# Kernel tuning notes

Measured on AMD Instinct MI355X. Metric: run time of the kernel, lower is better.

Reference implementation:

```python
import jax, jax.numpy as jnp
import numpy as np

VOCAB = 100000
EMB = 300
B, L = 2048, 256

def setup_inputs() -> dict:
    key = jax.random.key(0)
    k1, k2, k3, k4 = jax.random.split(key, 4)
    tokens = jax.random.randint(k1, (B, L), 0, VOCAB)
    # lengths in [1, L] (original items always have at least one token)
    lengths = jax.random.randint(k2, (B,), 1, L + 1)
    W_emb = jax.random.normal(k3, (VOCAB, EMB), dtype=jnp.float32)
    fc_w = jax.random.normal(k4, (1, EMB), dtype=jnp.float32) / np.sqrt(EMB)
    fc_b = jnp.zeros((1,), dtype=jnp.float32)
    return {"tokens": tokens, "lengths": lengths, "W_emb": W_emb, "fc_w": fc_w, "fc_b": fc_b}

def reference(tokens, lengths, W_emb, fc_w, fc_b):
    # ragged gather + per-item mean pool, fused via padding mask
    emb = W_emb[tokens]                                   # [B, L, D]
    mask = (jnp.arange(L)[None, :] < lengths[:, None])    # [B, L]
    summed = jnp.einsum('bld,bl->bd', emb, mask.astype(emb.dtype))
    avg = summed / lengths[:, None].astype(emb.dtype)     # [B, D]
    z = avg @ fc_w.T + fc_b                               # [B, 1]
    return jax.nn.sigmoid(z)
```

## Files before the change

### kernel.cpp

```cpp
#include <hip/hip_runtime.h>
#include <hip/hip_bf16.h>

#define VOCAB 100000
#define EMB 300
#define BATCH 2048
#define SEQ 256

__global__ void __launch_bounds__(256) vocab_dot_kernel(
    const float* __restrict__ W, const float* __restrict__ fcw,
    float* __restrict__ p, int nrows) {
  const int lane = threadIdx.x & 63;
  const int wave = (blockIdx.x * blockDim.x + threadIdx.x) >> 6;
  const int nwaves = (gridDim.x * blockDim.x) >> 6;

  const float4* fcw4 = (const float4*)fcw;
  float4 wa = fcw4[lane];
  float4 wb = make_float4(0.f, 0.f, 0.f, 0.f);
  if (lane < 11) wb = fcw4[64 + lane];

  for (int v = wave * 2; v < nrows; v += nwaves * 2) {
    const float4* r0 = (const float4*)(W + (size_t)v * EMB);
    float4 a0 = r0[lane];
    float4 t0 = (lane < 11) ? r0[64 + lane] : make_float4(0.f, 0.f, 0.f, 0.f);
    float4 a1 = make_float4(0.f, 0.f, 0.f, 0.f);
    float4 t1 = make_float4(0.f, 0.f, 0.f, 0.f);
    const bool has1 = (v + 1) < nrows;
    if (has1) {
      const float4* r1 = (const float4*)(W + (size_t)(v + 1) * EMB);
      a1 = r1[lane];
      if (lane < 11) t1 = r1[64 + lane];
    }

    float acc0 = a0.x * wa.x + a0.y * wa.y + a0.z * wa.z + a0.w * wa.w
               + t0.x * wb.x + t0.y * wb.y + t0.z * wb.z + t0.w * wb.w;
    float acc1 = a1.x * wa.x + a1.y * wa.y + a1.z * wa.z + a1.w * wa.w
               + t1.x * wb.x + t1.y * wb.y + t1.z * wb.z + t1.w * wb.w;

    #pragma unroll
    for (int off = 32; off > 0; off >>= 1) {
      acc0 += __shfl_down(acc0, off, 64);
      acc1 += __shfl_down(acc1, off, 64);
    }
    if (lane == 0) {
      p[v] = acc0;
      if (has1) p[v + 1] = acc1;
    }
  }
}

__global__ void __launch_bounds__(256) pool_sigmoid_kernel(
    const int* __restrict__ tokens, const int* __restrict__ lengths,
    const float* __restrict__ p, const float* __restrict__ fcb,
    float* __restrict__ out, int L) {
  __shared__ float part[4];
  const int b = blockIdx.x;
  const int t = threadIdx.x;
  const int len = lengths[b];

  float acc = 0.f;
  if (t < len) acc = p[tokens[(size_t)b * L + t]];

  #pragma unroll
  for (int off = 32; off > 0; off >>= 1)
    acc += __shfl_down(acc, off, 64);

  const int lane = t & 63, w = t >> 6;
  if (lane == 0) part[w] = acc;
  __syncthreads();
  if (t == 0) {
    float s = part[0] + part[1] + part[2] + part[3];
    float z = s / (float)len + fcb[0];
    out[b] = 1.0f / (1.0f + expf(-z));
  }
}

extern "C" void kernel_launch(void* const* d_in, const int* in_sizes, int n_in,
                              void* d_out, int out_size, void* d_ws, size_t ws_size,
                              hipStream_t stream) {
  const int*   tokens  = (const int*)d_in[0];
  const int*   lengths = (const int*)d_in[1];
  const float* W_emb   = (const float*)d_in[2];
  const float* fc_w    = (const float*)d_in[3];
  const float* fc_b    = (const float*)d_in[4];
  float* out = (float*)d_out;
  float* p   = (float*)d_ws;

  vocab_dot_kernel<<<2048, 256, 0, stream>>>(W_emb, fc_w, p, VOCAB);

  pool_sigmoid_kernel<<<BATCH, 256, 0, stream>>>(
      tokens, lengths, p, fc_b, out, SEQ);
}
```

Measured before the change: 27.57 us.

## Process four vocab rows per wave with 16-lane groups and nontemporal loads

Each wave now splits into four 16-lane groups, and each group computes the dot product of one embedding row with fc_w. That replaces the old two-rows-per-wave mapping and its 6-step full-wave shuffle reductions with a 4-step 16-lane xor reduction. Each lane issues five 16-byte loads per row instead of one or two, and the loads are marked nontemporal so the streaming read of W does not pollute the cache. This raises memory-level parallelism per wave and cuts shuffle overhead. It adds more registers for the five weight vectors.

Result: faster. 26.92 us (-2.3%).

```diff
diff --git a/kernel.cpp b/kernel.cpp
--- a/kernel.cpp
+++ b/kernel.cpp
@@ -6,45 +6,43 @@
 #define BATCH 2048
 #define SEQ 256
 
+typedef float f4 __attribute__((ext_vector_type(4)));
+
 __global__ void __launch_bounds__(256) vocab_dot_kernel(
     const float* __restrict__ W, const float* __restrict__ fcw,
     float* __restrict__ p, int nrows) {
   const int lane = threadIdx.x & 63;
+  const int g    = lane >> 4;
+  const int i    = lane & 15;
   const int wave = (blockIdx.x * blockDim.x + threadIdx.x) >> 6;
   const int nwaves = (gridDim.x * blockDim.x) >> 6;
 
-  const float4* fcw4 = (const float4*)fcw;
-  float4 wa = fcw4[lane];
-  float4 wb = make_float4(0.f, 0.f, 0.f, 0.f);
-  if (lane < 11) wb = fcw4[64 + lane];
+  const f4* fcw4 = (const f4*)fcw;
+  const f4 zero = (f4){0.f, 0.f, 0.f, 0.f};
+  f4 w0 = fcw4[i];
+  f4 w1 = fcw4[i + 16];
+  f4 w2 = fcw4[i + 32];
+  f4 w3 = fcw4[i + 48];
+  f4 w4 = (i < 11) ? fcw4[i + 64] : zero;
 
-  for (int v = wave * 2; v < nrows; v += nwaves * 2) {
-    const float4* r0 = (const float4*)(W + (size_t)v * EMB);
-    float4 a0 = r0[lane];
-    float4 t0 = (lane < 11) ? r0[64 + lane] : make_float4(0.f, 0.f, 0.f, 0.f);
-    float4 a1 = make_float4(0.f, 0.f, 0.f, 0.f);
-    float4 t1 = make_float4(0.f, 0.f, 0.f, 0.f);
-    const bool has1 = (v + 1) < nrows;
-    if (has1) {
-      const float4* r1 = (const float4*)(W + (size_t)(v + 1) * EMB);
-      a1 = r1[lane];
-      if (lane < 11) t1 = r1[64 + lane];
+  for (int v0 = wave * 4; v0 < nrows; v0 += nwaves * 4) {
+    const int v = v0 + g;
+    float acc = 0.f;
+    if (v < nrows) {
+      const f4* r = (const f4*)(W + (size_t)v * EMB);
+      f4 a0 = __builtin_nontemporal_load(&r[i]);
+      f4 a1 = __builtin_nontemporal_load(&r[i + 16]);
+      f4 a2 = __builtin_nontemporal_load(&r[i + 32]);
+      f4 a3 = __builtin_nontemporal_load(&r[i + 48]);
+      f4 a4 = (i < 11) ? __builtin_nontemporal_load(&r[i + 64]) : zero;
+      f4 s = a0 * w0 + a1 * w1 + a2 * w2 + a3 * w3 + a4 * w4;
+      acc = s.x + s.y + s.z + s.w;
     }
-
-    float acc0 = a0.x * wa.x + a0.y * wa.y + a0.z * wa.z + a0.w * wa.w
-               + t0.x * wb.x + t0.y * wb.y + t0.z * wb.z + t0.w * wb.w;
-    float acc1 = a1.x * wa.x + a1.y * wa.y + a1.z * wa.z + a1.w * wa.w
-               + t1.x * wb.x + t1.y * wb.y + t1.z * wb.z + t1.w * wb.w;
-
-    #pragma unroll
-    for (int off = 32; off > 0; off >>= 1) {
-      acc0 += __shfl_down(acc0, off, 64);
-      acc1 += __shfl_down(acc1, off, 64);
-    }
-    if (lane == 0) {
-      p[v] = acc0;
-      if (has1) p[v + 1] = acc1;
-    }
+    acc += __shfl_xor(acc, 8, 16);
+    acc += __shfl_xor(acc, 4, 16);
+    acc += __shfl_xor(acc, 2, 16);
+    acc += __shfl_xor(acc, 1, 16);
+    if (i == 0 && v < nrows) p[v] = acc;
   }
 }
 
```
